# Kernel optimization log

Measured on AMD Instinct MI355X. Metric: run time of the kernel, lower is better.

Reference implementation:

```python
import jax, jax.numpy as jnp
import numpy as np


def _grouped_attn(q, k, v, mask, scale):
    # q: [T,H,D], k/v: [S,KH,D], mask: [T,S] or [KH,T,S] (True = visible)
    T, H, D = q.shape
    S, KH, _ = k.shape
    G = H // KH
    qg = q.reshape(T, KH, G, D)
    logits = jnp.einsum('tkgd,skd->kgts', qg, k) * scale
    if mask.ndim == 2:
        mask = jnp.broadcast_to(mask[None], (KH, T, S))
    logits = jnp.where(mask[:, None], logits, -1e30)
    p = jax.nn.softmax(logits, axis=-1)
    valid = mask.any(-1)  # [KH,T]: queries with at least one visible key
    p = jnp.where(valid[:, None, :, None], p, 0.0)
    o = jnp.einsum('kgts,skd->tkgd', p, v).reshape(T, H, D)
    return o, p


def setup_inputs() -> dict:
    key = jax.random.key(0)
    ks = jax.random.split(key, 4)
    T, H, KH, D = 2048, 16, 2, 128
    q = jax.random.normal(ks[0], (T, H, D), jnp.float32)
    k = jax.random.normal(ks[1], (T, KH, D), jnp.float32)
    v = jax.random.normal(ks[2], (T, KH, D), jnp.float32)
    w = jax.random.uniform(ks[3], (T, H, 3), jnp.float32)
    return dict(q=q, k=k, v=v, w=w, kernel_size=32, stride=16, block_size=64,
                top_n=16, num_init_blocks=1, num_local_blocks=2, window_size=512)


def reference(q, k, v, w, kernel_size, stride, block_size, top_n,
              num_init_blocks, num_local_blocks, window_size):
    T, H, D = q.shape
    KH = k.shape[1]
    scale = 1.0 / np.sqrt(D).astype(np.float32)
    t = jnp.arange(T)
    causal = t[None, :] <= t[:, None]  # [T,S]

    # ---- 1) compression: mean-pool overlapping windows of kernel_size / stride ----
    n_cmp = (T - kernel_size) // stride + 1
    starts = np.arange(n_cmp) * stride
    win_idx = starts[:, None] + np.arange(kernel_size)[None, :]  # [Ncmp,ks]
    cmp_k = k[win_idx].mean(axis=1)  # [Ncmp,KH,D]
    cmp_v = v[win_idx].mean(axis=1)
    j_end = jnp.asarray(starts) + kernel_size - 1
    cmp_mask = j_end[None, :] <= t[:, None]  # block fully in the past
    o_cmp, p_cmp = _grouped_attn(q, cmp_k, cmp_v, cmp_mask, scale)  # p_cmp [KH,G,T,Ncmp]

    # ---- 2) block selection from compressed attention probabilities ----
    n_blk = (T + block_size - 1) // block_size
    js, je = starts, starts + kernel_size
    bs_, be_ = np.arange(n_blk) * block_size, (np.arange(n_blk) + 1) * block_size
    M = jnp.asarray(((js[:, None] < be_[None, :]) & (bs_[None, :] < je[:, None])),
                    dtype=q.dtype)  # [Ncmp,Nblk] overlap indicator
    blk_score = jnp.einsum('kgtj,jb->ktb', p_cmp, M)  # sum over group heads

    b = jnp.arange(n_blk)
    t_blk = t // block_size
    forced = (b[None, :] < num_init_blocks) | \
             ((b[None, :] <= t_blk[:, None]) & (b[None, :] >= t_blk[:, None] - num_local_blocks + 1))
    blk_valid = (b[None, :] * block_size) <= t[:, None]
    score = jnp.where(forced[None], 1e30, blk_score)
    score = jnp.where(blk_valid[None], score, -1e30)
    _, idx = jax.lax.top_k(score, top_n)  # [KH,T,top_n]
    sel_blk = jax.nn.one_hot(idx, n_blk, dtype=q.dtype).sum(-2) > 0  # [KH,T,Nblk]

    # ---- 3) selected-block attention ----
    tok_sel = sel_blk[:, :, t // block_size]  # [KH,T,T]
    slc_mask = tok_sel & causal[None]
    o_slc, _ = _grouped_attn(q, k, v, slc_mask, scale)

    # ---- 4) sliding-window attention ----
    win_mask = causal & ((t[:, None] - t[None, :]) < window_size)
    o_win, _ = _grouped_attn(q, k, v, win_mask, scale)

    # ---- 5) gated combination ----
    o = w[..., 0:1] * o_cmp + w[..., 1:2] * o_slc + w[..., 2:3] * o_win
    return o
```

## Files before the change

### kernel.cpp

```cpp
#include <hip/hip_runtime.h>
#include <hip/hip_bf16.h>
#include <math.h>

#define T_ 2048
#define H_ 16
#define KH_ 2
#define G_ 8
#define D_ 128
#define NCMP 127
#define JP 128
#define NBLK 32
#define TOPN 16
#define WIN_ 512
#define SCALE 0.08838834764831845f
#define SCL2 (0.08838834764831845f * 1.4426950408889634f)
#define THR2 11.541560f

typedef __attribute__((ext_vector_type(8))) short short8;
typedef __attribute__((ext_vector_type(16))) float f32x16;

__device__ __forceinline__ unsigned short f2bf(float x) {
    union { float f; unsigned u; } c; c.f = x;
    unsigned u = c.u + 0x7fffu + ((c.u >> 16) & 1u);
    return (unsigned short)(u >> 16);
}
__device__ __forceinline__ float bf2f(unsigned short b) {
    union { unsigned u; float f; } c; c.u = (unsigned)b << 16; return c.f;
}
__device__ __forceinline__ float exp2_fast(float x) {
    float r;
    asm("v_exp_f32 %0, %1" : "=v"(r) : "v"(x));
    return r;
}

#define GLD16(gsrc, lds) \
    __builtin_amdgcn_global_load_lds( \
        (const __attribute__((address_space(1))) unsigned int*)(gsrc), \
        (__attribute__((address_space(3))) unsigned int*)(lds), 16, 0, 0)

__global__ __launch_bounds__(256) void prep_kv(
        const float* __restrict__ k, const float* __restrict__ v,
        unsigned short* __restrict__ kimg, unsigned short* __restrict__ vtimg) {
    const int b  = blockIdx.x;
    const int kh = blockIdx.y;
    const int s0 = b << 6;
    const int tid = threadIdx.x;
    const size_t tb = ((size_t)kh * 32 + b) * 8192;
#pragma unroll
    for (int it = 0; it < 4; ++it) {
        int idx = it * 256 + tid;
        int r = idx >> 4, c = idx & 15;
        const float* src = k + (size_t)(s0 + r) * (KH_ * D_) + kh * D_ + c * 8;
        float4 x = *reinterpret_cast<const float4*>(src);
        float4 y = *reinterpret_cast<const float4*>(src + 4);
        union { unsigned short u[8]; uint4 q; } o;
        o.u[0] = f2bf(x.x); o.u[1] = f2bf(x.y); o.u[2] = f2bf(x.z); o.u[3] = f2bf(x.w);
        o.u[4] = f2bf(y.x); o.u[5] = f2bf(y.y); o.u[6] = f2bf(y.z); o.u[7] = f2bf(y.w);
        *reinterpret_cast<uint4*>(&kimg[tb + r * 128 + ((c ^ (r & 7)) << 3)]) = o.q;
    }
#pragma unroll
    for (int it = 0; it < 4; ++it) {
        int idx = it * 256 + tid;
        int d = idx & 127, kc8 = idx >> 7;
        union { unsigned short u[8]; uint4 q; } o;
#pragma unroll
        for (int e = 0; e < 8; ++e)
            o.u[e] = f2bf(v[(size_t)(s0 + kc8 * 8 + e) * (KH_ * D_) + kh * D_ + d]);
        *reinterpret_cast<uint4*>(&vtimg[tb + d * 64 + ((kc8 ^ (d & 7)) << 3)]) = o.q;
    }
}

__global__ __launch_bounds__(128) void build_cmp(
        const float* __restrict__ k, const float* __restrict__ v,
        unsigned short* __restrict__ khiI, unsigned short* __restrict__ kloI,
        unsigned short* __restrict__ vflat) {
    int j  = blockIdx.x;
    int kh = blockIdx.y;
    int d  = threadIdx.x;
    unsigned short hb = 0, lb = 0, vb = 0;
    if (j < NCMP) {
        int s0 = j * 16;
        float sk = 0.f, sv = 0.f;
        for (int i = 0; i < 32; ++i) {
            sk += k[(size_t)(s0 + i) * KH_ * D_ + kh * D_ + d];
            sv += v[(size_t)(s0 + i) * KH_ * D_ + kh * D_ + d];
        }
        float mk = sk * (1.f / 32.f), mv = sv * (1.f / 32.f);
        hb = f2bf(mk);
        lb = f2bf(mk - bf2f(hb));
        vb = f2bf(mv);
    }
    int c = d >> 3;
    size_t ib = (size_t)kh * 16384 + j * 128 + ((c ^ (j & 7)) << 3) + (d & 7);
    khiI[ib] = hb;
    kloI[ib] = lb;
    vflat[(size_t)kh * 16384 + j * 128 + d] = vb;
}

__global__ __launch_bounds__(256) void prep_cmp_img(
        const unsigned short* __restrict__ vflat, unsigned short* __restrict__ cvtI) {
    const int kh = blockIdx.x;
    const int tid = threadIdx.x;
#pragma unroll
    for (int it = 0; it < 8; ++it) {
        int idx = it * 256 + tid;
        int d = idx & 127, jc8 = idx >> 7;
        union { unsigned short u[8]; uint4 q; } o;
#pragma unroll
        for (int e = 0; e < 8; ++e)
            o.u[e] = vflat[(size_t)kh * 16384 + (jc8 * 8 + e) * 128 + d];
        *reinterpret_cast<uint4*>(
            &cvtI[(size_t)kh * 16384 + d * 128 + ((jc8 ^ (d & 7)) << 3)]) = o.q;
    }
}

__global__ __launch_bounds__(256, 1) void cmp_attn_mfma(
        const float* __restrict__ q, const float* __restrict__ w,
        const unsigned short* __restrict__ khiI, const unsigned short* __restrict__ kloI,
        const unsigned short* __restrict__ cvtI,
        float* __restrict__ out, unsigned int* __restrict__ sel) {
    const int qt  = blockIdx.x;
    const int kh  = blockIdx.y;
    const int t0  = qt * 16;
    const int tid = threadIdx.x;
    const int wv  = tid >> 6;
    const int lane = tid & 63;
    const int l31 = lane & 31;
    const int hi  = lane >> 5;
    const int hi4 = hi * 4;

    __shared__ unsigned short KHI[JP * D_];
    __shared__ unsigned short KLO[JP * D_];
    __shared__ unsigned short CVT[JP * D_];
    __shared__ float wsc_s[16 * 132];
    __shared__ float bsc_s[16 * 32];
    __shared__ unsigned int sel_s[16];
    __shared__ float wfac[4][32];

    if (tid < 16) sel_s[tid] = 0u;
    for (int i = tid; i < 16 * 132; i += 256) wsc_s[i] = 0.f;

    const size_t cb = (size_t)kh * 16384;
#pragma unroll
    for (int it = 0; it < 8; ++it) {
        int off = (wv * 8 + it) * 512;
        GLD16(khiI + cb + off + lane * 8, &KHI[off]);
        GLD16(kloI + cb + off + lane * 8, &KLO[off]);
        GLD16(cvtI + cb + off + lane * 8, &CVT[off]);
    }

    const int qloc = l31 & 15;
    const int t    = t0 + qloc;
    const int h    = kh * G_ + 2 * wv + (l31 >> 4);
    short8 qhi[8], qlo[8];
    {
        const float* qrow = q + (size_t)t * (H_ * D_) + h * D_;
#pragma unroll
        for (int dc = 0; dc < 8; ++dc) {
            int d0 = dc * 16 + hi * 8;
            float4 x = *reinterpret_cast<const float4*>(qrow + d0);
            float4 y = *reinterpret_cast<const float4*>(qrow + d0 + 4);
            float e_[8] = {x.x, x.y, x.z, x.w, y.x, y.y, y.z, y.w};
            short8 fh, fl;
#pragma unroll
            for (int e = 0; e < 8; ++e) {
                unsigned short hb = f2bf(e_[e]);
                fh[e] = (short)hb;
                fl[e] = (short)f2bf(e_[e] - bf2f(hb));
            }
            qhi[dc] = fh; qlo[dc] = fl;
        }
    }
    __syncthreads();

    f32x16 s_[4];
#pragma unroll
    for (int tl = 0; tl < 4; ++tl)
#pragma unroll
        for (int r = 0; r < 16; ++r) s_[tl][r] = 0.f;
    __builtin_amdgcn_s_setprio(1);
#pragma unroll
    for (int dc = 0; dc < 8; ++dc) {
        int c8 = dc * 2 + hi;
        int swz = (c8 ^ (l31 & 7)) << 3;
#pragma unroll
        for (int tl = 0; tl < 4; ++tl) {
            int off = (tl * 32 + l31) * 128 + swz;
            short8 ahi = *reinterpret_cast<const short8*>(&KHI[off]);
            short8 alo = *reinterpret_cast<const short8*>(&KLO[off]);
            s_[tl] = __builtin_amdgcn_mfma_f32_32x32x16_bf16(ahi, qhi[dc], s_[tl], 0, 0, 0);
            s_[tl] = __builtin_amdgcn_mfma_f32_32x32x16_bf16(alo, qhi[dc], s_[tl], 0, 0, 0);
            s_[tl] = __builtin_amdgcn_mfma_f32_32x32x16_bf16(ahi, qlo[dc], s_[tl], 0, 0, 0);
        }
    }
    __builtin_amdgcn_s_setprio(0);

    const int nv = (t >= 31) ? (((t - 31) >> 4) + 1) : 0;
    float m = -1e30f;
#pragma unroll
    for (int tl = 0; tl < 4; ++tl)
#pragma unroll
        for (int r = 0; r < 16; ++r) {
            int j = tl * 32 + (r & 3) + 8 * (r >> 2) + hi4;
            float lg = (j < nv) ? s_[tl][r] * SCALE : -1e30f;
            s_[tl][r] = lg;
            m = fmaxf(m, lg);
        }
    m = fmaxf(m, __shfl_xor(m, 32));
    float lsum = 0.f;
#pragma unroll
    for (int tl = 0; tl < 4; ++tl)
#pragma unroll
        for (int r = 0; r < 16; ++r) {
            float e = __expf(s_[tl][r] - m);
            s_[tl][r] = e;
            lsum += e;
        }
    lsum += __shfl_xor(lsum, 32);
    const float linv = (nv > 0) ? 1.f / lsum : 0.f;

#pragma unroll
    for (int tl = 0; tl < 4; ++tl)
#pragma unroll
        for (int r = 0; r < 16; ++r) {
            int j = tl * 32 + (r & 3) + 8 * (r >> 2) + hi4;
            atomicAdd(&wsc_s[qloc * 132 + j], s_[tl][r] * linv);
        }

    f32x16 acc[4];
#pragma unroll
    for (int dt = 0; dt < 4; ++dt)
#pragma unroll
        for (int r = 0; r < 16; ++r) acc[dt][r] = 0.f;
#pragma unroll
    for (int kc = 0; kc < 8; ++kc) {
        const int su = kc >> 1, rb = (kc & 1) * 8;
        unsigned pa0, pa1, pb0, pb1;
        asm("v_cvt_pk_bf16_f32 %0, %1, %2" : "=v"(pa0) : "v"(s_[su][rb+0]), "v"(s_[su][rb+1]));
        asm("v_cvt_pk_bf16_f32 %0, %1, %2" : "=v"(pa1) : "v"(s_[su][rb+2]), "v"(s_[su][rb+3]));
        asm("v_cvt_pk_bf16_f32 %0, %1, %2" : "=v"(pb0) : "v"(s_[su][rb+4]), "v"(s_[su][rb+5]));
        asm("v_cvt_pk_bf16_f32 %0, %1, %2" : "=v"(pb1) : "v"(s_[su][rb+6]), "v"(s_[su][rb+7]));
        unsigned sa0 = __shfl_xor(pa0, 32);
        unsigned sa1 = __shfl_xor(pa1, 32);
        unsigned sb0 = __shfl_xor(pb0, 32);
        unsigned sb1 = __shfl_xor(pb1, 32);
        union { unsigned u[4]; short8 s8; } pa;
        pa.u[0] = hi ? sb0 : pa0;
        pa.u[1] = hi ? sb1 : pa1;
        pa.u[2] = hi ? pb0 : sa0;
        pa.u[3] = hi ? pb1 : sa1;
        const int jc8 = kc * 2 + hi;
        __builtin_amdgcn_s_setprio(1);
#pragma unroll
        for (int dt = 0; dt < 4; ++dt) {
            int d = dt * 32 + l31;
            short8 bf = *reinterpret_cast<const short8*>(
                &CVT[d * 128 + ((jc8 ^ (d & 7)) << 3)]);
            acc[dt] = __builtin_amdgcn_mfma_f32_32x32x16_bf16(pa.s8, bf, acc[dt], 0, 0, 0);
        }
        __builtin_amdgcn_s_setprio(0);
    }

    wfac[wv][l31] = w[(size_t)t * (H_ * 3) + h * 3 + 0] * linv;
    __syncthreads();

    float wfr[16];
#pragma unroll
    for (int r = 0; r < 16; ++r)
        wfr[r] = wfac[wv][(r & 3) + 8 * (r >> 2) + hi4];
#pragma unroll
    for (int dt = 0; dt < 4; ++dt)
#pragma unroll
        for (int r = 0; r < 16; ++r) {
            int crow = (r & 3) + 8 * (r >> 2) + hi4;
            int tt = t0 + (crow & 15);
            int hh = kh * G_ + 2 * wv + (crow >> 4);
            out[(size_t)tt * (H_ * D_) + hh * D_ + dt * 32 + l31] = acc[dt][r] * wfr[r];
        }

#pragma unroll
    for (int half = 0; half < 2; ++half) {
        int b  = (tid & 15) + half * 16;
        int qq = tid >> 4;
        int tt = t0 + qq;
        float sc = 0.f;
        int j0 = 4 * b - 1; if (j0 < 0) j0 = 0;
        int j1 = 4 * b + 3; if (j1 > NCMP - 1) j1 = NCMP - 1;
        for (int j = j0; j <= j1; ++j) sc += wsc_s[qq * 132 + j];
        int tb = tt >> 6;
        bool forced = (b == 0) || (b <= tb && b >= tb - 1);
        if (forced) sc = 1e30f;
        if (b * 64 > tt) sc = -1e30f;
        bsc_s[qq * 32 + b] = sc;
    }
    __syncthreads();

#pragma unroll
    for (int half = 0; half < 2; ++half) {
        int b  = (tid & 15) + half * 16;
        int qq = tid >> 4;
        float sb = bsc_s[qq * 32 + b];
        int cnt = 0;
        for (int b2 = 0; b2 < NBLK; ++b2) {
            float s2 = bsc_s[qq * 32 + b2];
            cnt += (s2 > sb) || (s2 == sb && b2 < b);
        }
        if (cnt < TOPN) atomicOr(&sel_s[qq], 1u << b);
    }
    __syncthreads();
    if (tid < 16) sel[kh * T_ + t0 + tid] = sel_s[tid];
}

__global__ __launch_bounds__(128, 2) void slc_win_mfma(
        const float* __restrict__ q, const unsigned short* __restrict__ kimg,
        const unsigned short* __restrict__ vtimg, const float* __restrict__ w,
        const unsigned int* __restrict__ sel, float* __restrict__ out,
        float* __restrict__ winb, float* __restrict__ slcb, int use_scratch) {
    const int phase = blockIdx.z >> 1;
    const int hpair = blockIdx.z & 1;
    const int qt    = phase ? ((int)gridDim.x - 1 - (int)blockIdx.x) : (int)blockIdx.x;
    const int kh    = blockIdx.y;
    const int t0    = qt * 16;
    const int tid   = threadIdx.x;
    const int wv    = tid >> 6;
    const int lane  = tid & 63;
    const int l31   = lane & 31;
    const int hi    = lane >> 5;
    const int hi4   = hi * 4;

    __shared__ unsigned short Kl[64 * 128];
    __shared__ unsigned short Vt[128 * 64];
    __shared__ float wfac[2][32];

    const int qloc = l31 & 15;
    const int t    = t0 + qloc;
    const int hloc = hpair * 4 + wv * 2 + (l31 >> 4);
    const int h    = kh * G_ + hloc;

    short8 qf[8];
    {
        const float* qrow = q + (size_t)t * (H_ * D_) + h * D_;
#pragma unroll
        for (int dc = 0; dc < 8; ++dc) {
            int d0 = dc * 16 + hi * 8;
            float4 x = *reinterpret_cast<const float4*>(qrow + d0);
            float4 y = *reinterpret_cast<const float4*>(qrow + d0 + 4);
            short8 f;
            f[0] = (short)f2bf(x.x * SCL2); f[1] = (short)f2bf(x.y * SCL2);
            f[2] = (short)f2bf(x.z * SCL2); f[3] = (short)f2bf(x.w * SCL2);
            f[4] = (short)f2bf(y.x * SCL2); f[5] = (short)f2bf(y.y * SCL2);
            f[6] = (short)f2bf(y.z * SCL2); f[7] = (short)f2bf(y.w * SCL2);
            qf[dc] = f;
        }
    }

    const unsigned int smask = sel[kh * T_ + t];
    const int tbmax = t0 >> 6;
    unsigned int rem = 0;
    int bidx = 0;
    if (phase == 0) {
        int lo = t0 - (WIN_ - 1); if (lo < 0) lo = 0;
        bidx = lo >> 6;
    } else {
        unsigned int vm = (tbmax >= 31) ? 0xffffffffu : ((2u << tbmax) - 1u);
        rem = smask;
        rem |= __shfl_xor(rem, 1); rem |= __shfl_xor(rem, 2);
        rem |= __shfl_xor(rem, 4); rem |= __shfl_xor(rem, 8);
        rem &= vm;
    }

    f32x16 acc[4];
#pragma unroll
    for (int dt = 0; dt < 4; ++dt)
#pragma unroll
        for (int r = 0; r < 16; ++r) acc[dt][r] = 0.f;
    float m_run = -1e30f, l_run = 0.f;

    int b_cur;
    if (phase == 0) b_cur = bidx++;
    else { b_cur = rem ? (__ffs(rem) - 1) : -1; if (rem) rem &= rem - 1; }

    while (b_cur >= 0) {
        __syncthreads();
        {
            const size_t tb = ((size_t)kh * 32 + b_cur) * 8192;
#pragma unroll
            for (int it = 0; it < 8; ++it) {
                int off = (wv * 8 + it) * 512;
                GLD16(kimg + tb + off + lane * 8, &Kl[off]);
            }
#pragma unroll
            for (int it = 0; it < 8; ++it) {
                int off = (wv * 8 + it) * 512;
                GLD16(vtimg + tb + off + lane * 8, &Vt[off]);
            }
        }
        __syncthreads();

        const int s0 = b_cur << 6;

        f32x16 s_[2];
#pragma unroll
        for (int r = 0; r < 16; ++r) { s_[0][r] = 0.f; s_[1][r] = 0.f; }
        __builtin_amdgcn_s_setprio(1);
#pragma unroll
        for (int dc = 0; dc < 8; ++dc) {
            int c8 = dc * 2 + hi;
            int swz = (c8 ^ (l31 & 7)) << 3;
            short8 a0 = *reinterpret_cast<const short8*>(&Kl[l31 * 128 + swz]);
            short8 a1 = *reinterpret_cast<const short8*>(&Kl[(32 + l31) * 128 + swz]);
            s_[0] = __builtin_amdgcn_mfma_f32_32x32x16_bf16(a0, qf[dc], s_[0], 0, 0, 0);
            s_[1] = __builtin_amdgcn_mfma_f32_32x32x16_bf16(a1, qf[dc], s_[1], 0, 0, 0);
        }
        __builtin_amdgcn_s_setprio(0);

        const int sb = (smask >> b_cur) & 1;
        const bool needmask = (b_cur == tbmax) ||
                              ((phase == 0) && (s0 + 496 < t0));
        float mc = -1e30f;
        if (needmask) {
#pragma unroll
            for (int sub = 0; sub < 2; ++sub)
#pragma unroll
                for (int r = 0; r < 16; ++r) {
                    int crow = (r & 3) + 8 * (r >> 2) + hi4;
                    int s = s0 + sub * 32 + crow;
                    bool ok = (s <= t) && (phase ? (sb != 0) : (s + WIN_ > t));
                    float lg = ok ? s_[sub][r] : -1e30f;
                    s_[sub][r] = lg;
                    mc = fmaxf(mc, lg);
                }
        } else {
#pragma unroll
            for (int sub = 0; sub < 2; ++sub)
#pragma unroll
                for (int r = 0; r < 16; ++r) mc = fmaxf(mc, s_[sub][r]);
            if (phase) mc = sb ? mc : -1e30f;
        }

        float f = 1.f;
        const bool resc = !__all(mc <= m_run + THR2);
        if (resc) {
            float wm = mc;
            wm = fmaxf(wm, __shfl_xor(wm, 1));
            wm = fmaxf(wm, __shfl_xor(wm, 2));
            wm = fmaxf(wm, __shfl_xor(wm, 4));
            wm = fmaxf(wm, __shfl_xor(wm, 8));
            wm = fmaxf(wm, __shfl_xor(wm, 16));
            wm = fmaxf(wm, __shfl_xor(wm, 32));
            float mnew = fmaxf(m_run, wm);
            f = exp2_fast(m_run - mnew);
            m_run = mnew;
        }

        float lsum = 0.f;
#pragma unroll
        for (int sub = 0; sub < 2; ++sub)
#pragma unroll
            for (int r = 0; r < 16; ++r) {
                float e = exp2_fast(s_[sub][r] - m_run);
                s_[sub][r] = e;
                lsum += e;
            }
        if (phase && !sb) lsum = 0.f;
        lsum += __shfl_xor(lsum, 32);
        if (resc) {
            l_run = l_run * f + lsum;
#pragma unroll
            for (int dt = 0; dt < 4; ++dt)
#pragma unroll
                for (int r = 0; r < 16; ++r) acc[dt][r] *= f;
        } else {
            l_run += lsum;
        }

        const unsigned zm = (phase && !sb) ? 0u : 0xffffffffu;
#pragma unroll
        for (int kc = 0; kc < 4; ++kc) {
            const int su = kc >> 1, rb = (kc & 1) * 8;
            unsigned pa0, pb0, pa1, pb1;
            asm("v_cvt_pk_bf16_f32 %0, %1, %2" : "=v"(pa0) : "v"(s_[su][rb+0]), "v"(s_[su][rb+1]));
            asm("v_cvt_pk_bf16_f32 %0, %1, %2" : "=v"(pa1) : "v"(s_[su][rb+2]), "v"(s_[su][rb+3]));
            asm("v_cvt_pk_bf16_f32 %0, %1, %2" : "=v"(pb0) : "v"(s_[su][rb+4]), "v"(s_[su][rb+5]));
            asm("v_cvt_pk_bf16_f32 %0, %1, %2" : "=v"(pb1) : "v"(s_[su][rb+6]), "v"(s_[su][rb+7]));
            unsigned sa0 = __shfl_xor(pa0, 32);
            unsigned sa1 = __shfl_xor(pa1, 32);
            unsigned sb0 = __shfl_xor(pb0, 32);
            unsigned sb1 = __shfl_xor(pb1, 32);
            union { unsigned u[4]; short8 s8; } pa;
            pa.u[0] = (hi ? sb0 : pa0) & zm;
            pa.u[1] = (hi ? sb1 : pa1) & zm;
            pa.u[2] = (hi ? pb0 : sa0) & zm;
            pa.u[3] = (hi ? pb1 : sa1) & zm;
            const int kc8 = kc * 2 + hi;
            __builtin_amdgcn_s_setprio(1);
#pragma unroll
            for (int dt = 0; dt < 4; ++dt) {
                int d = dt * 32 + l31;
                short8 bf = *reinterpret_cast<const short8*>(
                    &Vt[d * 64 + ((kc8 ^ (d & 7)) << 3)]);
                acc[dt] = __builtin_amdgcn_mfma_f32_32x32x16_bf16(pa.s8, bf, acc[dt], 0, 0, 0);
            }
            __builtin_amdgcn_s_setprio(0);
        }

        if (phase == 0) b_cur = (bidx <= tbmax) ? bidx++ : -1;
        else { b_cur = rem ? (__ffs(rem) - 1) : -1; if (rem) rem &= rem - 1; }
    }

    float linv = 1.f / l_run;
    int widx = (phase == 0) ? 2 : 1;
    wfac[wv][l31] = w[(size_t)t * (H_ * 3) + h * 3 + widx] * linv;
    __syncthreads();
    float wfr[16];
#pragma unroll
    for (int r = 0; r < 16; ++r)
        wfr[r] = wfac[wv][(r & 3) + 8 * (r >> 2) + hi4];
    float* base = (phase == 0) ? winb : slcb;
#pragma unroll
    for (int dt = 0; dt < 4; ++dt)
#pragma unroll
        for (int r = 0; r < 16; ++r) {
            int crow = (r & 3) + 8 * (r >> 2) + hi4;
            int tt = t0 + (crow & 15);
            int hh = kh * G_ + hpair * 4 + wv * 2 + (crow >> 4);
            size_t idx = (size_t)tt * (H_ * D_) + hh * D_ + dt * 32 + l31;
            float val = acc[dt][r] * wfr[r];
            if (use_scratch) base[idx] = val;
            else             atomicAdd(&out[idx], val);
        }
}

__global__ __launch_bounds__(256) void combine_out(float* __restrict__ out,
        const float* __restrict__ a, const float* __restrict__ b) {
    int i = blockIdx.x * 256 + threadIdx.x;
    float4 o = reinterpret_cast<float4*>(out)[i];
    float4 x = reinterpret_cast<const float4*>(a)[i];
    float4 y = reinterpret_cast<const float4*>(b)[i];
    o.x += x.x + y.x; o.y += x.y + y.y; o.z += x.z + y.z; o.w += x.w + y.w;
    reinterpret_cast<float4*>(out)[i] = o;
}

extern "C" void kernel_launch(void* const* d_in, const int* in_sizes, int n_in,
                              void* d_out, int out_size, void* d_ws, size_t ws_size,
                              hipStream_t stream) {
    const float* q = (const float*)d_in[0];
    const float* k = (const float*)d_in[1];
    const float* v = (const float*)d_in[2];
    const float* w = (const float*)d_in[3];
    float* out = (float*)d_out;

    char* ws = (char*)d_ws;
    unsigned short* kimg  = (unsigned short*)(ws);
    unsigned short* vtimg = (unsigned short*)(ws + (1u << 20));
    unsigned short* khiI  = (unsigned short*)(ws + (2u << 20));
    unsigned short* kloI  = (unsigned short*)(ws + (2u << 20) + 65536);
    unsigned short* cvtI  = (unsigned short*)(ws + (2u << 20) + 2 * 65536);
    unsigned short* vflat = (unsigned short*)(ws + (2u << 20) + 3 * 65536);
    unsigned int*   sel   = (unsigned int*)(ws + (2u << 20) + 4 * 65536);
    float* winb_s = (float*)(ws + (2u << 20) + 4 * 65536 + 16384);
    float* slcb_s = winb_s + (size_t)T_ * H_ * D_;
    const size_t need = (2u << 20) + 4 * 65536 + 16384
                        + 2 * (size_t)T_ * H_ * D_ * sizeof(float);
    const int use_scratch = (ws_size >= need) ? 1 : 0;
    float* winb = use_scratch ? winb_s : out;
    float* slcb = use_scratch ? slcb_s : out;

    hipLaunchKernelGGL(prep_kv, dim3(32, KH_), dim3(256), 0, stream, k, v, kimg, vtimg);
    hipLaunchKernelGGL(build_cmp, dim3(128, KH_), dim3(128), 0, stream,
                       k, v, khiI, kloI, vflat);
    hipLaunchKernelGGL(prep_cmp_img, dim3(KH_), dim3(256), 0, stream, vflat, cvtI);
    hipLaunchKernelGGL(cmp_attn_mfma, dim3(T_ / 16, KH_), dim3(256), 0, stream,
                       q, w, khiI, kloI, cvtI, out, sel);
    hipLaunchKernelGGL(slc_win_mfma, dim3(T_ / 16, KH_, 4), dim3(128), 0, stream,
                       q, kimg, vtimg, w, sel, out, winb, slcb, use_scratch);
    if (use_scratch) {
        hipLaunchKernelGGL(combine_out, dim3((T_ * H_ * D_ / 4) / 256), dim3(256), 0, stream,
                           out, winb, slcb);
    }
}
```

Baseline: 226.4 us.

## Read MFMA operands directly from global fragment layouts instead of LDS staging

The K/V and compressed K/V images are re-laid out into MFMA fragment-major order so each lane loads its short8 operand straight from global memory (through L1/L2). This drops the LDS copies, barriers and setprio in both attention kernels, and removes the prep_cmp_img kernel by writing the transposed compressed V directly. The slc/win kernel now uses 256-thread blocks covering all 8 group heads instead of two 128-thread head-pair blocks, and the LDS weight broadcast becomes a wavefront shuffle. The cost is more global/L2 traffic for operands that were previously shared through LDS, plus exposed load latency without explicit staging.

```diff
diff --git a/kernel.cpp b/kernel.cpp
--- a/kernel.cpp
+++ b/kernel.cpp
@@ -33,11 +33,6 @@
     return r;
 }
 
-#define GLD16(gsrc, lds) \
-    __builtin_amdgcn_global_load_lds( \
-        (const __attribute__((address_space(1))) unsigned int*)(gsrc), \
-        (__attribute__((address_space(3))) unsigned int*)(lds), 16, 0, 0)
-
 __global__ __launch_bounds__(256) void prep_kv(
         const float* __restrict__ k, const float* __restrict__ v,
         unsigned short* __restrict__ kimg, unsigned short* __restrict__ vtimg) {
@@ -56,7 +51,7 @@
         union { unsigned short u[8]; uint4 q; } o;
         o.u[0] = f2bf(x.x); o.u[1] = f2bf(x.y); o.u[2] = f2bf(x.z); o.u[3] = f2bf(x.w);
         o.u[4] = f2bf(y.x); o.u[5] = f2bf(y.y); o.u[6] = f2bf(y.z); o.u[7] = f2bf(y.w);
-        *reinterpret_cast<uint4*>(&kimg[tb + r * 128 + ((c ^ (r & 7)) << 3)]) = o.q;
+        *reinterpret_cast<uint4*>(&kimg[tb + c * 512 + r * 8]) = o.q;
     }
 #pragma unroll
     for (int it = 0; it < 4; ++it) {
@@ -66,14 +61,14 @@
 #pragma unroll
         for (int e = 0; e < 8; ++e)
             o.u[e] = f2bf(v[(size_t)(s0 + kc8 * 8 + e) * (KH_ * D_) + kh * D_ + d]);
-        *reinterpret_cast<uint4*>(&vtimg[tb + d * 64 + ((kc8 ^ (d & 7)) << 3)]) = o.q;
+        *reinterpret_cast<uint4*>(&vtimg[tb + kc8 * 1024 + d * 8]) = o.q;
     }
 }
 
 __global__ __launch_bounds__(128) void build_cmp(
         const float* __restrict__ k, const float* __restrict__ v,
-        unsigned short* __restrict__ khiI, unsigned short* __restrict__ kloI,
-        unsigned short* __restrict__ vflat) {
+        unsigned short* __restrict__ khiF, unsigned short* __restrict__ kloF,
+        unsigned short* __restrict__ cvtF) {
     int j  = blockIdx.x;
     int kh = blockIdx.y;
     int d  = threadIdx.x;
@@ -90,34 +85,17 @@
         lb = f2bf(mk - bf2f(hb));
         vb = f2bf(mv);
     }
-    int c = d >> 3;
-    size_t ib = (size_t)kh * 16384 + j * 128 + ((c ^ (j & 7)) << 3) + (d & 7);
-    khiI[ib] = hb;
-    kloI[ib] = lb;
-    vflat[(size_t)kh * 16384 + j * 128 + d] = vb;
-}
-
-__global__ __launch_bounds__(256) void prep_cmp_img(
-        const unsigned short* __restrict__ vflat, unsigned short* __restrict__ cvtI) {
-    const int kh = blockIdx.x;
-    const int tid = threadIdx.x;
-#pragma unroll
-    for (int it = 0; it < 8; ++it) {
-        int idx = it * 256 + tid;
-        int d = idx & 127, jc8 = idx >> 7;
-        union { unsigned short u[8]; uint4 q; } o;
-#pragma unroll
-        for (int e = 0; e < 8; ++e)
-            o.u[e] = vflat[(size_t)kh * 16384 + (jc8 * 8 + e) * 128 + d];
-        *reinterpret_cast<uint4*>(
-            &cvtI[(size_t)kh * 16384 + d * 128 + ((jc8 ^ (d & 7)) << 3)]) = o.q;
-    }
+    size_t base = (size_t)kh * 16384;
+    size_t ib = base + (d >> 3) * 1024 + j * 8 + (d & 7);
+    khiF[ib] = hb;
+    kloF[ib] = lb;
+    cvtF[base + (j >> 3) * 1024 + d * 8 + (j & 7)] = vb;
 }
 
 __global__ __launch_bounds__(256, 1) void cmp_attn_mfma(
         const float* __restrict__ q, const float* __restrict__ w,
-        const unsigned short* __restrict__ khiI, const unsigned short* __restrict__ kloI,
-        const unsigned short* __restrict__ cvtI,
+        const unsigned short* __restrict__ khiF, const unsigned short* __restrict__ kloF,
+        const unsigned short* __restrict__ cvtF,
         float* __restrict__ out, unsigned int* __restrict__ sel) {
     const int qt  = blockIdx.x;
     const int kh  = blockIdx.y;
@@ -129,25 +107,17 @@
     const int hi  = lane >> 5;
     const int hi4 = hi * 4;
 
-    __shared__ unsigned short KHI[JP * D_];
-    __shared__ unsigned short KLO[JP * D_];
-    __shared__ unsigned short CVT[JP * D_];
     __shared__ float wsc_s[16 * 132];
     __shared__ float bsc_s[16 * 32];
     __shared__ unsigned int sel_s[16];
-    __shared__ float wfac[4][32];
 
     if (tid < 16) sel_s[tid] = 0u;
     for (int i = tid; i < 16 * 132; i += 256) wsc_s[i] = 0.f;
-
-    const size_t cb = (size_t)kh * 16384;
-#pragma unroll
-    for (int it = 0; it < 8; ++it) {
-        int off = (wv * 8 + it) * 512;
-        GLD16(khiI + cb + off + lane * 8, &KHI[off]);
-        GLD16(kloI + cb + off + lane * 8, &KLO[off]);
-        GLD16(cvtI + cb + off + lane * 8, &CVT[off]);
-    }
+    __syncthreads();
+
+    const unsigned short* KH = khiF + (size_t)kh * 16384;
+    const unsigned short* KL = kloF + (size_t)kh * 16384;
+    const unsigned short* CV = cvtF + (size_t)kh * 16384;
 
     const int qloc = l31 & 15;
     const int t    = t0 + qloc;
@@ -171,29 +141,25 @@
             qhi[dc] = fh; qlo[dc] = fl;
         }
     }
-    __syncthreads();
 
     f32x16 s_[4];
 #pragma unroll
     for (int tl = 0; tl < 4; ++tl)
 #pragma unroll
         for (int r = 0; r < 16; ++r) s_[tl][r] = 0.f;
-    __builtin_amdgcn_s_setprio(1);
 #pragma unroll
     for (int dc = 0; dc < 8; ++dc) {
-        int c8 = dc * 2 + hi;
-        int swz = (c8 ^ (l31 & 7)) << 3;
+        int base = (dc * 2 + hi) * 1024 + l31 * 8;
 #pragma unroll
         for (int tl = 0; tl < 4; ++tl) {
-            int off = (tl * 32 + l31) * 128 + swz;
-            short8 ahi = *reinterpret_cast<const short8*>(&KHI[off]);
-            short8 alo = *reinterpret_cast<const short8*>(&KLO[off]);
+            int off = base + tl * 256;
+            short8 ahi = *reinterpret_cast<const short8*>(&KH[off]);
+            short8 alo = *reinterpret_cast<const short8*>(&KL[off]);
             s_[tl] = __builtin_amdgcn_mfma_f32_32x32x16_bf16(ahi, qhi[dc], s_[tl], 0, 0, 0);
             s_[tl] = __builtin_amdgcn_mfma_f32_32x32x16_bf16(alo, qhi[dc], s_[tl], 0, 0, 0);
             s_[tl] = __builtin_amdgcn_mfma_f32_32x32x16_bf16(ahi, qlo[dc], s_[tl], 0, 0, 0);
         }
     }
-    __builtin_amdgcn_s_setprio(0);
 
     const int nv = (t >= 31) ? (((t - 31) >> 4) + 1) : 0;
     float m = -1e30f;
@@ -250,24 +216,19 @@
         pa.u[2] = hi ? pb0 : sa0;
         pa.u[3] = hi ? pb1 : sa1;
         const int jc8 = kc * 2 + hi;
-        __builtin_amdgcn_s_setprio(1);
 #pragma unroll
         for (int dt = 0; dt < 4; ++dt) {
             int d = dt * 32 + l31;
-            short8 bf = *reinterpret_cast<const short8*>(
-                &CVT[d * 128 + ((jc8 ^ (d & 7)) << 3)]);
+            short8 bf = *reinterpret_cast<const short8*>(&CV[jc8 * 1024 + d * 8]);
             acc[dt] = __builtin_amdgcn_mfma_f32_32x32x16_bf16(pa.s8, bf, acc[dt], 0, 0, 0);
         }
-        __builtin_amdgcn_s_setprio(0);
-    }
-
-    wfac[wv][l31] = w[(size_t)t * (H_ * 3) + h * 3 + 0] * linv;
-    __syncthreads();
-
+    }
+
+    float wfacv = w[(size_t)t * (H_ * 3) + h * 3 + 0] * linv;
     float wfr[16];
 #pragma unroll
     for (int r = 0; r < 16; ++r)
-        wfr[r] = wfac[wv][(r & 3) + 8 * (r >> 2) + hi4];
+        wfr[r] = __shfl(wfacv, (r & 3) + 8 * (r >> 2) + hi4);
 #pragma unroll
     for (int dt = 0; dt < 4; ++dt)
 #pragma unroll
@@ -277,6 +238,8 @@
             int hh = kh * G_ + 2 * wv + (crow >> 4);
             out[(size_t)tt * (H_ * D_) + hh * D_ + dt * 32 + l31] = acc[dt][r] * wfr[r];
         }
+
+    __syncthreads();
 
 #pragma unroll
     for (int half = 0; half < 2; ++half) {
@@ -311,13 +274,12 @@
     if (tid < 16) sel[kh * T_ + t0 + tid] = sel_s[tid];
 }
 
-__global__ __launch_bounds__(128, 2) void slc_win_mfma(
+__global__ __launch_bounds__(256, 2) void slc_win_mfma(
         const float* __restrict__ q, const unsigned short* __restrict__ kimg,
         const unsigned short* __restrict__ vtimg, const float* __restrict__ w,
         const unsigned int* __restrict__ sel, float* __restrict__ out,
         float* __restrict__ winb, float* __restrict__ slcb, int use_scratch) {
-    const int phase = blockIdx.z >> 1;
-    const int hpair = blockIdx.z & 1;
+    const int phase = blockIdx.z;
     const int qt    = phase ? ((int)gridDim.x - 1 - (int)blockIdx.x) : (int)blockIdx.x;
     const int kh    = blockIdx.y;
     const int t0    = qt * 16;
@@ -328,14 +290,9 @@
     const int hi    = lane >> 5;
     const int hi4   = hi * 4;
 
-    __shared__ unsigned short Kl[64 * 128];
-    __shared__ unsigned short Vt[128 * 64];
-    __shared__ float wfac[2][32];
-
     const int qloc = l31 & 15;
     const int t    = t0 + qloc;
-    const int hloc = hpair * 4 + wv * 2 + (l31 >> 4);
-    const int h    = kh * G_ + hloc;
+    const int h    = kh * G_ + 2 * wv + (l31 >> 4);
 
     short8 qf[8];
     {
@@ -381,38 +338,21 @@
     else { b_cur = rem ? (__ffs(rem) - 1) : -1; if (rem) rem &= rem - 1; }
 
     while (b_cur >= 0) {
-        __syncthreads();
-        {
-            const size_t tb = ((size_t)kh * 32 + b_cur) * 8192;
-#pragma unroll
-            for (int it = 0; it < 8; ++it) {
-                int off = (wv * 8 + it) * 512;
-                GLD16(kimg + tb + off + lane * 8, &Kl[off]);
-            }
-#pragma unroll
-            for (int it = 0; it < 8; ++it) {
-                int off = (wv * 8 + it) * 512;
-                GLD16(vtimg + tb + off + lane * 8, &Vt[off]);
-            }
-        }
-        __syncthreads();
-
         const int s0 = b_cur << 6;
+        const unsigned short* Kt = kimg  + ((size_t)kh * 32 + b_cur) * 8192;
+        const unsigned short* Vt = vtimg + ((size_t)kh * 32 + b_cur) * 8192;
 
         f32x16 s_[2];
 #pragma unroll
         for (int r = 0; r < 16; ++r) { s_[0][r] = 0.f; s_[1][r] = 0.f; }
-        __builtin_amdgcn_s_setprio(1);
 #pragma unroll
         for (int dc = 0; dc < 8; ++dc) {
-            int c8 = dc * 2 + hi;
-            int swz = (c8 ^ (l31 & 7)) << 3;
-            short8 a0 = *reinterpret_cast<const short8*>(&Kl[l31 * 128 + swz]);
-            short8 a1 = *reinterpret_cast<const short8*>(&Kl[(32 + l31) * 128 + swz]);
+            int base = (dc * 2 + hi) * 512 + l31 * 8;
+            short8 a0 = *reinterpret_cast<const short8*>(&Kt[base]);
+            short8 a1 = *reinterpret_cast<const short8*>(&Kt[base + 256]);
             s_[0] = __builtin_amdgcn_mfma_f32_32x32x16_bf16(a0, qf[dc], s_[0], 0, 0, 0);
             s_[1] = __builtin_amdgcn_mfma_f32_32x32x16_bf16(a1, qf[dc], s_[1], 0, 0, 0);
         }
-        __builtin_amdgcn_s_setprio(0);
 
         const int sb = (smask >> b_cur) & 1;
         const bool needmask = (b_cur == tbmax) ||
@@ -493,15 +433,12 @@
             pa.u[2] = (hi ? pb0 : sa0) & zm;
             pa.u[3] = (hi ? pb1 : sa1) & zm;
             const int kc8 = kc * 2 + hi;
-            __builtin_amdgcn_s_setprio(1);
 #pragma unroll
             for (int dt = 0; dt < 4; ++dt) {
                 int d = dt * 32 + l31;
-                short8 bf = *reinterpret_cast<const short8*>(
-                    &Vt[d * 64 + ((kc8 ^ (d & 7)) << 3)]);
+                short8 bf = *reinterpret_cast<const short8*>(&Vt[kc8 * 1024 + d * 8]);
                 acc[dt] = __builtin_amdgcn_mfma_f32_32x32x16_bf16(pa.s8, bf, acc[dt], 0, 0, 0);
             }
-            __builtin_amdgcn_s_setprio(0);
         }
 
         if (phase == 0) b_cur = (bidx <= tbmax) ? bidx++ : -1;
@@ -510,12 +447,11 @@
 
     float linv = 1.f / l_run;
     int widx = (phase == 0) ? 2 : 1;
-    wfac[wv][l31] = w[(size_t)t * (H_ * 3) + h * 3 + widx] * linv;
-    __syncthreads();
+    float wfacv = w[(size_t)t * (H_ * 3) + h * 3 + widx] * linv;
     float wfr[16];
 #pragma unroll
     for (int r = 0; r < 16; ++r)
-        wfr[r] = wfac[wv][(r & 3) + 8 * (r >> 2) + hi4];
+        wfr[r] = __shfl(wfacv, (r & 3) + 8 * (r >> 2) + hi4);
     float* base = (phase == 0) ? winb : slcb;
 #pragma unroll
     for (int dt = 0; dt < 4; ++dt)
@@ -523,7 +459,7 @@
         for (int r = 0; r < 16; ++r) {
             int crow = (r & 3) + 8 * (r >> 2) + hi4;
             int tt = t0 + (crow & 15);
-            int hh = kh * G_ + hpair * 4 + wv * 2 + (crow >> 4);
+            int hh = kh * G_ + 2 * wv + (crow >> 4);
             size_t idx = (size_t)tt * (H_ * D_) + hh * D_ + dt * 32 + l31;
             float val = acc[dt][r] * wfr[r];
             if (use_scratch) base[idx] = val;
@@ -553,14 +489,13 @@
     char* ws = (char*)d_ws;
     unsigned short* kimg  = (unsigned short*)(ws);
     unsigned short* vtimg = (unsigned short*)(ws + (1u << 20));
-    unsigned short* khiI  = (unsigned short*)(ws + (2u << 20));
-    unsigned short* kloI  = (unsigned short*)(ws + (2u << 20) + 65536);
-    unsigned short* cvtI  = (unsigned short*)(ws + (2u << 20) + 2 * 65536);
-    unsigned short* vflat = (unsigned short*)(ws + (2u << 20) + 3 * 65536);
-    unsigned int*   sel   = (unsigned int*)(ws + (2u << 20) + 4 * 65536);
-    float* winb_s = (float*)(ws + (2u << 20) + 4 * 65536 + 16384);
+    unsigned short* khiF  = (unsigned short*)(ws + (2u << 20));
+    unsigned short* kloF  = (unsigned short*)(ws + (2u << 20) + 65536);
+    unsigned short* cvtF  = (unsigned short*)(ws + (2u << 20) + 2 * 65536);
+    unsigned int*   sel   = (unsigned int*)(ws + (2u << 20) + 3 * 65536);
+    float* winb_s = (float*)(ws + (2u << 20) + 3 * 65536 + 16384);
     float* slcb_s = winb_s + (size_t)T_ * H_ * D_;
-    const size_t need = (2u << 20) + 4 * 65536 + 16384
+    const size_t need = (2u << 20) + 3 * 65536 + 16384
                         + 2 * (size_t)T_ * H_ * D_ * sizeof(float);
     const int use_scratch = (ws_size >= need) ? 1 : 0;
     float* winb = use_scratch ? winb_s : out;
@@ -568,11 +503,10 @@
 
     hipLaunchKernelGGL(prep_kv, dim3(32, KH_), dim3(256), 0, stream, k, v, kimg, vtimg);
     hipLaunchKernelGGL(build_cmp, dim3(128, KH_), dim3(128), 0, stream,
-                       k, v, khiI, kloI, vflat);
-    hipLaunchKernelGGL(prep_cmp_img, dim3(KH_), dim3(256), 0, stream, vflat, cvtI);
+                       k, v, khiF, kloF, cvtF);
     hipLaunchKernelGGL(cmp_attn_mfma, dim3(T_ / 16, KH_), dim3(256), 0, stream,
-                       q, w, khiI, kloI, cvtI, out, sel);
-    hipLaunchKernelGGL(slc_win_mfma, dim3(T_ / 16, KH_, 4), dim3(128), 0, stream,
+                       q, w, khiF, kloF, cvtF, out, sel);
+    hipLaunchKernelGGL(slc_win_mfma, dim3(T_ / 16, KH_, 2), dim3(256), 0, stream,
                        q, kimg, vtimg, w, sel, out, winb, slcb, use_scratch);
     if (use_scratch) {
         hipLaunchKernelGGL(combine_out, dim3((T_ * H_ * D_ / 4) / 256), dim3(256), 0, stream,
```

Result: slower. 266.8 us (+17.9%).
